# Kernel tuning notes

Measured on AMD Instinct MI355X. Metric: run time of the kernel, lower is better.

## Reference

```python
import jax, jax.numpy as jnp
import numpy as np

IN_F, OUT_F, RANK, ALPHA, NUM_ADAPTERS = 1024, 1024, 8, 1.0, 8
B, S = 32, 1024
SCALE = ALPHA / RANK


def setup_inputs() -> dict:
    key = jax.random.key(0)
    k1, k2, k3, k4, k5, k6 = jax.random.split(key, 6)
    x = jax.random.normal(k1, (B, S, IN_F), dtype=jnp.float32)
    subject_id = jax.random.randint(k2, (B,), 0, NUM_ADAPTERS)
    # base linear: W [out,in], bias [out] (torch nn.Linear layout)
    W = jax.random.normal(k3, (OUT_F, IN_F), dtype=jnp.float32) * (1.0 / np.sqrt(IN_F))
    b = jax.random.normal(k4, (OUT_F,), dtype=jnp.float32) * 0.01
    # stacked LoRA weights: A [E, rank, in], Bw [E, out, rank]
    # (original inits Bw to zeros; randomized here so the LoRA path is exercised)
    A = jax.random.normal(k5, (NUM_ADAPTERS, RANK, IN_F), dtype=jnp.float32) * 0.02
    Bw = jax.random.normal(k6, (NUM_ADAPTERS, OUT_F, RANK), dtype=jnp.float32) * 0.02
    return {"x": x, "W": W, "b": b, "A": A, "Bw": Bw, "subject_id": subject_id}


def reference(x, W, b, A, Bw, subject_id):
    # base linear: [B,S,O]
    out = jnp.einsum("bsd,od->bso", x, W) + b
    # gather per-batch adapter weights (equivalent to the per-adapter mask loop)
    A_sel = A[subject_id]   # [B, rank, in]
    B_sel = Bw[subject_id]  # [B, out, rank]
    h = jnp.einsum("bsd,brd->bsr", x, A_sel)          # [B,S,rank]
    lora = jnp.einsum("bsr,bor->bso", h, B_sel) * SCALE  # [B,S,out]
    return out + lora
```

## Files before the change

kernel.cpp:

```cpp
#include <hip/hip_runtime.h>
#include <hip/hip_bf16.h>

typedef __bf16 bf16_t;
typedef bf16_t bf16x4 __attribute__((ext_vector_type(4)));
typedef bf16_t bf16x8 __attribute__((ext_vector_type(8)));
typedef float  f32x4  __attribute__((ext_vector_type(4)));

#define IN_F   1024
#define OUT_F  1024
#define RANK   8
#define NE     8
#define BATCH  32
#define SEQ    1024
#define M_TOT  (BATCH * SEQ)
#define SCALE  0.125f
#define NT     16

#define GLOAD_LDS16(g, l)                                                     \
  __builtin_amdgcn_global_load_lds(                                           \
      (const __attribute__((address_space(1))) void*)(g),                     \
      (__attribute__((address_space(3))) void*)(l), 16, 0, 0)

#define CFENCE asm volatile("" ::: "memory")
#define BAR()                                                                 \
  do { CFENCE; __builtin_amdgcn_s_barrier(); CFENCE; } while (0)
#define VMCNT(n) asm volatile("s_waitcnt vmcnt(" #n ")" ::: "memory")

__global__ __launch_bounds__(256) void build_frag(
    const float* __restrict__ W, const float* __restrict__ A,
    const float* __restrict__ Bw, bf16_t* __restrict__ wfrag) {
  const int wid = threadIdx.x >> 6, lane = threadIdx.x & 63;
  const int L = (blockIdx.x << 2) + wid;
  const int e  = L >> 11;
  const int nb = (L >> 9) & 3;
  const int kt = (L >> 5) & 15;
  const int kh = (L >> 4) & 1;
  const int wn = (L >> 2) & 3;
  const int ni = L & 3;
  const int o  = (nb << 8) + (wn << 6) + (ni << 4) + (lane & 15);
  const int kb = (kt << 6) + (kh << 5) + ((lane >> 4) << 3);

  const float* wrow = W + ((size_t)o << 10) + kb;
  f32x4 s0 = *(const f32x4*)(wrow);
  f32x4 s1 = *(const f32x4*)(wrow + 4);
  const float* bwr = Bw + ((((size_t)e << 10) + o) << 3);
  const float* ab  = A + (((size_t)e << 3) << 10) + kb;
#pragma unroll
  for (int r = 0; r < RANK; ++r) {
    const float c = SCALE * bwr[r];
    s0 += c * *(const f32x4*)(ab + ((size_t)r << 10));
    s1 += c * *(const f32x4*)(ab + ((size_t)r << 10) + 4);
  }
  bf16x8 v;
#pragma unroll
  for (int j = 0; j < 4; ++j) { v[j] = (bf16_t)s0[j]; v[4 + j] = (bf16_t)s1[j]; }
  *(bf16x8*)(wfrag + ((size_t)L << 9) + (lane << 3)) = v;
}

__global__ __launch_bounds__(256) void cvt_x(const float* __restrict__ x,
                                             bf16_t* __restrict__ xb, int n4) {
  int i = blockIdx.x * 256 + threadIdx.x;
  const int stride = gridDim.x * 256;
  for (; i < n4; i += stride) {
    const f32x4 v = *(const f32x4*)(x + ((size_t)i << 2));
    bf16x4 o;
#pragma unroll
    for (int j = 0; j < 4; ++j) o[j] = (bf16_t)v[j];
    *(bf16x4*)(xb + ((size_t)i << 2)) = o;
  }
}

__global__ __launch_bounds__(512, 2) void gemm256(
    const bf16_t* __restrict__ xb, const bf16_t* __restrict__ wfrag,
    const float* __restrict__ bias, const int* __restrict__ sid,
    float* __restrict__ out) {
  __shared__ bf16_t lds_a[2][2][8192];

  const int bid0 = blockIdx.x;
  const int wgid = ((bid0 & 7) << 6) + (bid0 >> 3);
  const int mb = wgid >> 2, nb = wgid & 3;
  const int m0 = mb << 8;
  const int e = sid[mb >> 2];

  const int tid = threadIdx.x;
  const int lane = tid & 63, wid = tid >> 6;
  const int wm = wid >> 2, wn = wid & 3;

  const bf16_t* agbase = xb + ((size_t)m0 << 10);
  const bf16_t* bgf = wfrag + ((((size_t)e << 2) + nb) << 18) + (wn << 11) +
                      (lane << 3);

  int soff[2];
#pragma unroll
  for (int i = 0; i < 2; ++i) {
    const int r = (wid << 5) + (i << 4) + (lane >> 2);
    const int sg = (lane & 3) ^ ((r >> 1) & 3);
    soff[i] = (r << 10) + (sg << 3);
  }
  int aoff[8];
#pragma unroll
  for (int mi = 0; mi < 8; ++mi) {
    const int r = (wm << 7) + (mi << 4) + (lane & 15);
    const int g = (lane >> 4) ^ ((r >> 1) & 3);
    aoff[mi] = (r << 5) + (g << 3);
  }

  f32x4 acc[8][4] = {};
  bf16x8 af[8], bfr[2][2][4];

#define ASTG(kt, c)                                                           \
  do {                                                                        \
    const int _k0 = (kt) << 6;                                                \
    bf16_t* _d0 = &lds_a[c][0][wid << 10];                                    \
    bf16_t* _d1 = &lds_a[c][1][wid << 10];                                    \
    GLOAD_LDS16(agbase + _k0 + soff[0], _d0);                                 \
    GLOAD_LDS16(agbase + _k0 + soff[1], _d0 + 512);                           \
    GLOAD_LDS16(agbase + _k0 + 32 + soff[0], _d1);                            \
    GLOAD_LDS16(agbase + _k0 + 32 + soff[1], _d1 + 512);                      \
  } while (0)

#define BLOAD(kt, S)                                                          \
  do {                                                                        \
    const bf16_t* _p = bgf + ((size_t)(kt) << 14);                            \
    _Pragma("unroll") for (int _n = 0; _n < 4; ++_n)                          \
        bfr[S][0][_n] = *(const bf16x8*)(_p + (_n << 9));                     \
    _Pragma("unroll") for (int _n = 0; _n < 4; ++_n)                          \
        bfr[S][1][_n] = *(const bf16x8*)(_p + 8192 + (_n << 9));              \
  } while (0)

#define RD(c, kh)                                                             \
  do {                                                                        \
    const bf16_t* _ab = &lds_a[c][kh][0];                                     \
    _Pragma("unroll") for (int mi = 0; mi < 8; ++mi)                          \
        af[mi] = *(const bf16x8*)(_ab + aoff[mi]);                            \
  } while (0)

#define MM(S, kh)                                                             \
  do {                                                                        \
    __builtin_amdgcn_s_setprio(1);                                            \
    _Pragma("unroll") for (int mi = 0; mi < 8; ++mi)                          \
        _Pragma("unroll") for (int ni = 0; ni < 4; ++ni)                      \
            acc[mi][ni] = __builtin_amdgcn_mfma_f32_16x16x32_bf16(            \
                af[mi], bfr[S][kh][ni], acc[mi][ni], 0, 0, 0);                \
    __builtin_amdgcn_s_setprio(0);                                            \
  } while (0)

#define TILE(J, C, S, NXT, DO_ISSUE)                                          \
  do {                                                                        \
    RD(C, 0);                                                                 \
    if (DO_ISSUE) { BLOAD((J) + 1, NXT); ASTG((J) + 1, 1 - (C)); }            \
    MM(S, 0);                                                                 \
    RD(C, 1);                                                                 \
    MM(S, 1);                                                                 \
    if (DO_ISSUE) { VMCNT(0); BAR(); }                                        \
  } while (0)

  BLOAD(0, 0);
  ASTG(0, 0);
  VMCNT(0);
  BAR();

  for (int jj = 0; jj < 7; ++jj) {
    const int j0 = jj << 1;
    TILE(j0, 0, 0, 1, 1);
    TILE(j0 + 1, 1, 1, 0, 1);
  }
  TILE(14, 0, 0, 1, 1);
  TILE(15, 1, 1, 0, 0);

  const int R0 = m0 + (wm << 7);
  const int C0 = (nb << 8) + (wn << 6);
  const int crow = (lane >> 4) << 2;
  const int ccol = lane & 15;
#pragma unroll
  for (int ni = 0; ni < 4; ++ni) {
    const int col = C0 + (ni << 4) + ccol;
    const float bv = bias[col];
#pragma unroll
    for (int mi = 0; mi < 8; ++mi) {
      const int row = R0 + (mi << 4) + crow;
#pragma unroll
      for (int j2 = 0; j2 < 4; ++j2)
        out[((size_t)(row + j2) << 10) + col] = acc[mi][ni][j2] + bv;
    }
  }
#undef ASTG
#undef BLOAD
#undef RD
#undef MM
#undef TILE
}

__global__ __launch_bounds__(256) void lora_naive(
    const float* __restrict__ x, const float* __restrict__ W,
    const float* __restrict__ bias, const float* __restrict__ A,
    const float* __restrict__ Bw, const int* __restrict__ sid,
    float* __restrict__ out) {
  const int m = blockIdx.x;
  const int e = sid[m >> 10];
  __shared__ float xs[IN_F];
  __shared__ float h[RANK];
  const int tid = threadIdx.x;
  for (int i = tid; i < IN_F; i += 256) xs[i] = x[((size_t)m << 10) + i];
  __syncthreads();
  if (tid < RANK) {
    float s = 0.f;
    const float* ar = A + (((size_t)e * RANK + tid) << 10);
    for (int d = 0; d < IN_F; ++d) s += xs[d] * ar[d];
    h[tid] = s * SCALE;
  }
  __syncthreads();
  for (int o = tid; o < OUT_F; o += 256) {
    const float* wr = W + ((size_t)o << 10);
    float s = 0.f;
    for (int d = 0; d < IN_F; ++d) s += xs[d] * wr[d];
    const float* bwr = Bw + (((size_t)e << 10) + o) * RANK;
    float l = 0.f;
#pragma unroll
    for (int r = 0; r < RANK; ++r) l += h[r] * bwr[r];
    out[((size_t)m << 10) + o] = s + bias[o] + l;
  }
}

extern "C" void kernel_launch(void* const* d_in, const int* in_sizes, int n_in,
                              void* d_out, int out_size, void* d_ws,
                              size_t ws_size, hipStream_t stream) {
  const float* x   = (const float*)d_in[0];
  const float* W   = (const float*)d_in[1];
  const float* b   = (const float*)d_in[2];
  const float* A   = (const float*)d_in[3];
  const float* Bw  = (const float*)d_in[4];
  const int*   sid = (const int*)d_in[5];
  float* out = (float*)d_out;

  const size_t wfrag_bytes = (size_t)NE * OUT_F * IN_F * 2;
  const size_t xb_bytes    = (size_t)M_TOT * IN_F * 2;

  if (ws_size >= wfrag_bytes + xb_bytes) {
    bf16_t* wfrag = (bf16_t*)d_ws;
    bf16_t* xb    = (bf16_t*)((char*)d_ws + wfrag_bytes);
    hipLaunchKernelGGL(build_frag, dim3(4096), dim3(256), 0, stream,
                       W, A, Bw, wfrag);
    hipLaunchKernelGGL(cvt_x, dim3(4096), dim3(256), 0, stream,
                       x, xb, M_TOT * IN_F / 4);
    hipLaunchKernelGGL(gemm256, dim3((M_TOT / 256) * (OUT_F / 256)),
                       dim3(512), 0, stream, xb, wfrag, b, sid, out);
  } else {
    hipLaunchKernelGGL(lora_naive, dim3(M_TOT), dim3(256), 0, stream,
                       x, W, b, A, Bw, sid, out);
  }
}
```

Baseline: 140.7 us.

## Fuse fp32-to-bf16 conversion of x into GEMM LDS staging

```diff
diff --git a/kernel.cpp b/kernel.cpp
--- a/kernel.cpp
+++ b/kernel.cpp
@@ -57,24 +57,11 @@
   *(bf16x8*)(wfrag + ((size_t)L << 9) + (lane << 3)) = v;
 }
 
-__global__ __launch_bounds__(256) void cvt_x(const float* __restrict__ x,
-                                             bf16_t* __restrict__ xb, int n4) {
-  int i = blockIdx.x * 256 + threadIdx.x;
-  const int stride = gridDim.x * 256;
-  for (; i < n4; i += stride) {
-    const f32x4 v = *(const f32x4*)(x + ((size_t)i << 2));
-    bf16x4 o;
-#pragma unroll
-    for (int j = 0; j < 4; ++j) o[j] = (bf16_t)v[j];
-    *(bf16x4*)(xb + ((size_t)i << 2)) = o;
-  }
-}
-
 __global__ __launch_bounds__(512, 2) void gemm256(
-    const bf16_t* __restrict__ xb, const bf16_t* __restrict__ wfrag,
+    const float* __restrict__ xf, const bf16_t* __restrict__ wfrag,
     const float* __restrict__ bias, const int* __restrict__ sid,
     float* __restrict__ out) {
-  __shared__ bf16_t lds_a[2][2][8192];
+  __shared__ float lds_af[2][16384];
 
   const int bid0 = blockIdx.x;
   const int wgid = ((bid0 & 7) << 6) + (bid0 >> 3);
@@ -86,37 +73,35 @@
   const int lane = tid & 63, wid = tid >> 6;
   const int wm = wid >> 2, wn = wid & 3;
 
-  const bf16_t* agbase = xb + ((size_t)m0 << 10);
+  const float* agf = xf + ((size_t)m0 << 10);
   const bf16_t* bgf = wfrag + ((((size_t)e << 2) + nb) << 18) + (wn << 11) +
                       (lane << 3);
 
   int soff[2];
 #pragma unroll
   for (int i = 0; i < 2; ++i) {
-    const int r = (wid << 5) + (i << 4) + (lane >> 2);
-    const int sg = (lane & 3) ^ ((r >> 1) & 3);
-    soff[i] = (r << 10) + (sg << 3);
+    const int r = (wid << 5) + (i << 2) + (lane >> 4);
+    const int g = ((lane & 15) >> 1) ^ (r & 7);
+    soff[i] = (r << 10) + (g << 3) + ((lane & 1) << 2);
   }
   int aoff[8];
 #pragma unroll
   for (int mi = 0; mi < 8; ++mi) {
     const int r = (wm << 7) + (mi << 4) + (lane & 15);
-    const int g = (lane >> 4) ^ ((r >> 1) & 3);
-    aoff[mi] = (r << 5) + (g << 3);
+    const int p = (lane >> 4) ^ (r & 7);
+    aoff[mi] = (r << 6) + (p << 3);
   }
 
   f32x4 acc[8][4] = {};
-  bf16x8 af[8], bfr[2][2][4];
+  bf16x8 bfr[2][2][4];
 
 #define ASTG(kt, c)                                                           \
   do {                                                                        \
-    const int _k0 = (kt) << 6;                                                \
-    bf16_t* _d0 = &lds_a[c][0][wid << 10];                                    \
-    bf16_t* _d1 = &lds_a[c][1][wid << 10];                                    \
-    GLOAD_LDS16(agbase + _k0 + soff[0], _d0);                                 \
-    GLOAD_LDS16(agbase + _k0 + soff[1], _d0 + 512);                           \
-    GLOAD_LDS16(agbase + _k0 + 32 + soff[0], _d1);                            \
-    GLOAD_LDS16(agbase + _k0 + 32 + soff[1], _d1 + 512);                      \
+    float* _d = &lds_af[c][wid << 11];                                        \
+    const int _k = (kt) << 6;                                                 \
+    _Pragma("unroll") for (int i = 0; i < 8; ++i)                             \
+        GLOAD_LDS16(agf + _k + soff[i & 1] + ((i >> 1) << 13),                \
+                    _d + (i << 8));                                           \
   } while (0)
 
 #define BLOAD(kt, S)                                                          \
@@ -128,30 +113,30 @@
         bfr[S][1][_n] = *(const bf16x8*)(_p + 8192 + (_n << 9));              \
   } while (0)
 
-#define RD(c, kh)                                                             \
-  do {                                                                        \
-    const bf16_t* _ab = &lds_a[c][kh][0];                                     \
-    _Pragma("unroll") for (int mi = 0; mi < 8; ++mi)                          \
-        af[mi] = *(const bf16x8*)(_ab + aoff[mi]);                            \
-  } while (0)
-
-#define MM(S, kh)                                                             \
-  do {                                                                        \
-    __builtin_amdgcn_s_setprio(1);                                            \
-    _Pragma("unroll") for (int mi = 0; mi < 8; ++mi)                          \
-        _Pragma("unroll") for (int ni = 0; ni < 4; ++ni)                      \
-            acc[mi][ni] = __builtin_amdgcn_mfma_f32_16x16x32_bf16(            \
-                af[mi], bfr[S][kh][ni], acc[mi][ni], 0, 0, 0);                \
-    __builtin_amdgcn_s_setprio(0);                                            \
+#define KSTEP(c, kh, S)                                                       \
+  do {                                                                        \
+    const float* _ab = &lds_af[c][0];                                         \
+    _Pragma("unroll") for (int mi = 0; mi < 8; ++mi) {                        \
+      const int _o = aoff[mi] ^ ((kh) << 5);                                  \
+      const f32x4 _lo = *(const f32x4*)(_ab + _o);                            \
+      const f32x4 _hi = *(const f32x4*)(_ab + _o + 4);                        \
+      bf16x8 _a8;                                                             \
+      _Pragma("unroll") for (int _j = 0; _j < 4; ++_j) {                      \
+        _a8[_j] = (bf16_t)_lo[_j]; _a8[4 + _j] = (bf16_t)_hi[_j];             \
+      }                                                                       \
+      __builtin_amdgcn_s_setprio(1);                                          \
+      _Pragma("unroll") for (int ni = 0; ni < 4; ++ni)                        \
+          acc[mi][ni] = __builtin_amdgcn_mfma_f32_16x16x32_bf16(              \
+              _a8, bfr[S][kh][ni], acc[mi][ni], 0, 0, 0);                     \
+      __builtin_amdgcn_s_setprio(0);                                          \
+    }                                                                         \
   } while (0)
 
 #define TILE(J, C, S, NXT, DO_ISSUE)                                          \
   do {                                                                        \
-    RD(C, 0);                                                                 \
     if (DO_ISSUE) { BLOAD((J) + 1, NXT); ASTG((J) + 1, 1 - (C)); }            \
-    MM(S, 0);                                                                 \
-    RD(C, 1);                                                                 \
-    MM(S, 1);                                                                 \
+    KSTEP(C, 0, S);                                                           \
+    KSTEP(C, 1, S);                                                           \
     if (DO_ISSUE) { VMCNT(0); BAR(); }                                        \
   } while (0)
 
@@ -186,8 +171,7 @@
   }
 #undef ASTG
 #undef BLOAD
-#undef RD
-#undef MM
+#undef KSTEP
 #undef TILE
 }
 
@@ -234,17 +218,13 @@
   float* out = (float*)d_out;
 
   const size_t wfrag_bytes = (size_t)NE * OUT_F * IN_F * 2;
-  const size_t xb_bytes    = (size_t)M_TOT * IN_F * 2;
-
-  if (ws_size >= wfrag_bytes + xb_bytes) {
+
+  if (ws_size >= wfrag_bytes) {
     bf16_t* wfrag = (bf16_t*)d_ws;
-    bf16_t* xb    = (bf16_t*)((char*)d_ws + wfrag_bytes);
     hipLaunchKernelGGL(build_frag, dim3(4096), dim3(256), 0, stream,
                        W, A, Bw, wfrag);
-    hipLaunchKernelGGL(cvt_x, dim3(4096), dim3(256), 0, stream,
-                       x, xb, M_TOT * IN_F / 4);
     hipLaunchKernelGGL(gemm256, dim3((M_TOT / 256) * (OUT_F / 256)),
-                       dim3(512), 0, stream, xb, wfrag, b, sid, out);
+                       dim3(512), 0, stream, x, wfrag, b, sid, out);
   } else {
     hipLaunchKernelGGL(lora_naive, dim3(M_TOT), dim3(256), 0, stream,
                        x, W, b, A, Bw, sid, out);
```

Result: faster. 134.8 us (-4.2%).
